# Optimization experiments

Hardware: AMD Instinct MI355X
Metric: run time of the kernel (lower is better)

The kernel has to match this reference:

```python
import jax, jax.numpy as jnp
import numpy as np

N_NODES = 100000
HID = 128
N_EDGES = 600000


def sage_conv(h, src, dst, Wl, bl, Wr, n_nodes):
    # PyG SAGEConv (mean aggr): out = lin_l(mean_{j->i} h_j) + lin_r(h_i)
    msgs = h[src]                                               # [E, d] gather
    agg = jax.ops.segment_sum(msgs, dst, num_segments=n_nodes)  # [N, d]
    cnt = jax.ops.segment_sum(jnp.ones((src.shape[0], 1), h.dtype), dst,
                              num_segments=n_nodes)             # [N, 1]
    mean = agg / jnp.maximum(cnt, 1.0)                          # isolated nodes -> 0
    return mean @ Wl.T + bl + h @ Wr.T


def setup_inputs() -> dict:
    key = jax.random.key(0)
    ks = jax.random.split(key, 8)
    scale = 1.0 / np.sqrt(HID)
    x = jnp.arange(N_NODES, dtype=jnp.int64) if jax.config.jax_enable_x64 else jnp.arange(N_NODES, dtype=jnp.int32)
    edge_index = jax.random.randint(ks[0], (2, N_EDGES), 0, N_NODES)
    emb = jax.random.normal(ks[1], (N_NODES, HID), dtype=jnp.float32) * scale
    Wl1 = jax.random.normal(ks[2], (HID, HID), dtype=jnp.float32) * scale
    bl1 = jnp.zeros((HID,), jnp.float32)
    Wr1 = jax.random.normal(ks[3], (HID, HID), dtype=jnp.float32) * scale
    Wl2 = jax.random.normal(ks[4], (HID, HID), dtype=jnp.float32) * scale
    bl2 = jnp.zeros((HID,), jnp.float32)
    Wr2 = jax.random.normal(ks[5], (HID, HID), dtype=jnp.float32) * scale
    return {"x": x, "edge_index": edge_index, "emb": emb,
            "Wl1": Wl1, "bl1": bl1, "Wr1": Wr1,
            "Wl2": Wl2, "bl2": bl2, "Wr2": Wr2}


def reference(x, edge_index, emb, Wl1, bl1, Wr1, Wl2, bl2, Wr2):
    src, dst = edge_index[0], edge_index[1]
    n = emb.shape[0]
    h = emb[x]                                          # embedding lookup [N, d]
    h = jax.nn.relu(sage_conv(h, src, dst, Wl1, bl1, Wr1, n))  # dropout = eval identity
    h = jax.nn.relu(sage_conv(h, src, dst, Wl2, bl2, Wr2, n))
    return h
```

## Files before the change

### kernel.cpp

```cpp
#include <hip/hip_runtime.h>

#define HID 128

typedef unsigned short ushort_t;
typedef unsigned int uint_t;
typedef float f32x4 __attribute__((ext_vector_type(4)));
typedef short s16x8 __attribute__((ext_vector_type(8)));

__device__ __forceinline__ ushort_t f2bf(float f) {
  uint_t u = __float_as_uint(f);
  uint_t r = (u + 0x7FFFu + ((u >> 16) & 1u)) >> 16;
  return (ushort_t)r;
}
__device__ __forceinline__ float bfLo(uint_t v) { return __uint_as_float(v << 16); }
__device__ __forceinline__ float bfHi(uint_t v) { return __uint_as_float(v & 0xFFFF0000u); }

__global__ __launch_bounds__(256) void prep_kernel(
    const float* __restrict__ emb, const int* __restrict__ x,
    ushort_t* __restrict__ hb, int N,
    const float* __restrict__ Wl1, const float* __restrict__ Wr1,
    const float* __restrict__ Wl2, const float* __restrict__ Wr2,
    ushort_t* __restrict__ wsw,
    const int* __restrict__ dst, int* __restrict__ deg, int E) {
  int tid = blockIdx.x * 256 + threadIdx.x;
  int gthreads = N * 32;
  if (tid < gthreads) {
    int r = tid >> 5, j = (tid & 31) * 4;
    int s = x[r];
    float4 v = *(const float4*)&emb[(size_t)s * HID + j];
    uint2 p;
    p.x = (uint_t)f2bf(v.x) | ((uint_t)f2bf(v.y) << 16);
    p.y = (uint_t)f2bf(v.z) | ((uint_t)f2bf(v.w) << 16);
    *(uint2*)&hb[(size_t)r * HID + j] = p;
    return;
  }
  tid -= gthreads;
  if (tid < 65536) {
    const float* srcs[4] = {Wl1, Wr1, Wl2, Wr2};
    int m = tid >> 14, idx = tid & 16383;
    int j = idx & 7;
    int lane = (idx >> 3) & 63;
    int nt = (idx >> 9) & 7;
    int ks = (idx >> 12) & 3;
    int row = nt * 16 + (lane & 15);
    int col = ks * 32 + (lane >> 4) * 8 + j;
    wsw[tid] = f2bf(srcs[m][row * HID + col]);
    return;
  }
  tid -= 65536;
  if (tid < E) atomicAdd(&deg[dst[tid]], 1);
}

__global__ __launch_bounds__(256) void scan1_kernel(
    const int* __restrict__ deg, int* __restrict__ offsets,
    int* __restrict__ sums, int N) {
  __shared__ int s[256];
  int b = blockIdx.x, t = threadIdx.x;
  int base = b * 1024 + t * 4;
  int v0 = 0, v1 = 0, v2 = 0, v3 = 0;
  if (base + 0 < N) v0 = deg[base + 0];
  if (base + 1 < N) v1 = deg[base + 1];
  if (base + 2 < N) v2 = deg[base + 2];
  if (base + 3 < N) v3 = deg[base + 3];
  int mySum = v0 + v1 + v2 + v3;
  s[t] = mySum;
  __syncthreads();
  for (int off = 1; off < 256; off <<= 1) {
    int v = (t >= off) ? s[t - off] : 0;
    __syncthreads();
    s[t] += v;
    __syncthreads();
  }
  int excl = s[t] - mySum;
  if (t == 255) sums[b] = s[255];
  if (base + 0 < N) offsets[base + 0] = excl;
  if (base + 1 < N) offsets[base + 1] = excl + v0;
  if (base + 2 < N) offsets[base + 2] = excl + v0 + v1;
  if (base + 3 < N) offsets[base + 3] = excl + v0 + v1 + v2;
}

__global__ __launch_bounds__(256) void scan3_kernel(
    int* __restrict__ offsets, const int* __restrict__ sums,
    int* __restrict__ cursor, int N, int E, int nb) {
  __shared__ int red[256];
  int t = threadIdx.x;
  int chunk = (blockIdx.x * 256) >> 10;
  red[t] = (t < chunk) ? sums[t] : 0;
  __syncthreads();
  for (int off = 128; off > 0; off >>= 1) {
    if (t < off) red[t] += red[t + off];
    __syncthreads();
  }
  int prefix = red[0];
  int i = blockIdx.x * 256 + t;
  if (i < N) {
    int v = offsets[i] + prefix;
    offsets[i] = v;
    cursor[i] = v;
  } else if (i == N) {
    offsets[N] = E;
  }
}

__global__ __launch_bounds__(256) void fill_kernel(
    const int* __restrict__ src, const int* __restrict__ dst,
    int* __restrict__ cursor, int* __restrict__ csr, int E) {
  int e = blockIdx.x * 256 + threadIdx.x;
  if (e >= E) return;
  int d = dst[e];
  int pos = atomicAdd(&cursor[d], 1);
  csr[pos] = src[e];
}

__global__ __launch_bounds__(256) void aggregate_kernel(
    const ushort_t* __restrict__ hb, const int* __restrict__ offsets,
    const int* __restrict__ csr, ushort_t* __restrict__ meanb, int N) {
  int t = threadIdx.x;
  int node = blockIdx.x * 4 + (t >> 6);
  if (node >= N) return;
  int lane = t & 63;
  int grp = lane >> 4;
  int l16 = lane & 15;
  int o0 = offsets[node], o1 = offsets[node + 1];

  float acc[8];
#pragma unroll
  for (int i = 0; i < 8; i++) acc[i] = 0.f;

  int e = o0 + grp;
  for (; e + 4 < o1; e += 8) {
    int s0 = csr[e];
    int s1 = csr[e + 4];
    uint4 v0 = *(const uint4*)&hb[(size_t)s0 * HID + l16 * 8];
    uint4 v1 = *(const uint4*)&hb[(size_t)s1 * HID + l16 * 8];
    acc[0] += bfLo(v0.x) + bfLo(v1.x);
    acc[1] += bfHi(v0.x) + bfHi(v1.x);
    acc[2] += bfLo(v0.y) + bfLo(v1.y);
    acc[3] += bfHi(v0.y) + bfHi(v1.y);
    acc[4] += bfLo(v0.z) + bfLo(v1.z);
    acc[5] += bfHi(v0.z) + bfHi(v1.z);
    acc[6] += bfLo(v0.w) + bfLo(v1.w);
    acc[7] += bfHi(v0.w) + bfHi(v1.w);
  }
  if (e < o1) {
    int s0 = csr[e];
    uint4 v0 = *(const uint4*)&hb[(size_t)s0 * HID + l16 * 8];
    acc[0] += bfLo(v0.x); acc[1] += bfHi(v0.x);
    acc[2] += bfLo(v0.y); acc[3] += bfHi(v0.y);
    acc[4] += bfLo(v0.z); acc[5] += bfHi(v0.z);
    acc[6] += bfLo(v0.w); acc[7] += bfHi(v0.w);
  }

#pragma unroll
  for (int i = 0; i < 8; i++) {
    acc[i] += __shfl_xor(acc[i], 16, 64);
    acc[i] += __shfl_xor(acc[i], 32, 64);
  }

  if (grp == 0) {
    int d = o1 - o0;
    float inv = 1.0f / (float)(d > 1 ? d : 1);
    uint4 p;
    p.x = (uint_t)f2bf(acc[0] * inv) | ((uint_t)f2bf(acc[1] * inv) << 16);
    p.y = (uint_t)f2bf(acc[2] * inv) | ((uint_t)f2bf(acc[3] * inv) << 16);
    p.z = (uint_t)f2bf(acc[4] * inv) | ((uint_t)f2bf(acc[5] * inv) << 16);
    p.w = (uint_t)f2bf(acc[6] * inv) | ((uint_t)f2bf(acc[7] * inv) << 16);
    *(uint4*)&meanb[(size_t)node * HID + l16 * 8] = p;
  }
}

__global__ __launch_bounds__(256) void mfma_gemm_kernel(
    const ushort_t* __restrict__ meanb, const ushort_t* __restrict__ hb,
    const ushort_t* __restrict__ WlS, const ushort_t* __restrict__ WrS,
    const float* __restrict__ bias, float* __restrict__ outF,
    ushort_t* __restrict__ outB, int N, int outIsBf16) {
  __shared__ ushort_t ws[32768];
  const int t = threadIdx.x;
  const int wave = t >> 6;
  const int lane = t & 63;
  const int rowBase = (blockIdx.x * 4 + wave) * 32;
  const int l15 = lane & 15;
  const int quad = lane >> 4;
  const int kq = quad * 8;
  const bool active = rowBase < N;

  int r0 = rowBase + l15;       if (r0 >= N) r0 = N - 1;
  int r1 = rowBase + 16 + l15;  if (r1 >= N) r1 = N - 1;

  s16x8 a[2][2][4];
  if (active) {
#pragma unroll
    for (int ks = 0; ks < 4; ks++) {
      a[0][0][ks] = *(const s16x8*)&meanb[(size_t)r0 * HID + ks * 32 + kq];
      a[0][1][ks] = *(const s16x8*)&meanb[(size_t)r1 * HID + ks * 32 + kq];
      a[1][0][ks] = *(const s16x8*)&hb[(size_t)r0 * HID + ks * 32 + kq];
      a[1][1][ks] = *(const s16x8*)&hb[(size_t)r1 * HID + ks * 32 + kq];
    }
  }

#pragma unroll
  for (int it = 0; it < 8; it++) {
    int o = (it * 256 + t) * 8;
    *(s16x8*)&ws[o] = *(const s16x8*)&WlS[o];
    *(s16x8*)&ws[16384 + o] = *(const s16x8*)&WrS[o];
  }
  __syncthreads();

  if (active) {
    f32x4 acc[2][8];
#pragma unroll
    for (int mt = 0; mt < 2; mt++)
#pragma unroll
      for (int nt = 0; nt < 8; nt++) acc[mt][nt] = (f32x4){0.f, 0.f, 0.f, 0.f};

#pragma unroll
    for (int half = 0; half < 2; half++) {
      const int hbase = half * 16384;
#pragma unroll
      for (int ks = 0; ks < 4; ks++)
#pragma unroll
        for (int nt = 0; nt < 8; nt++) {
          s16x8 b = *(const s16x8*)&ws[hbase + ((ks * 8 + nt) * 64 + lane) * 8];
          acc[0][nt] = __builtin_amdgcn_mfma_f32_16x16x32_bf16(a[half][0][ks], b, acc[0][nt], 0, 0, 0);
          acc[1][nt] = __builtin_amdgcn_mfma_f32_16x16x32_bf16(a[half][1][ks], b, acc[1][nt], 0, 0, 0);
        }
    }

#pragma unroll
    for (int mt = 0; mt < 2; mt++) {
#pragma unroll
      for (int nt = 0; nt < 8; nt++) {
        int col = nt * 16 + l15;
        float bv = bias[col];
#pragma unroll
        for (int r = 0; r < 4; r++) {
          int row = rowBase + mt * 16 + quad * 4 + r;
          if (row < N) {
            float v = fmaxf(acc[mt][nt][r] + bv, 0.f);
            if (outIsBf16) outB[(size_t)row * HID + col] = f2bf(v);
            else           outF[(size_t)row * HID + col] = v;
          }
        }
      }
    }
  }
}

extern "C" void kernel_launch(void* const* d_in, const int* in_sizes, int n_in,
                              void* d_out, int out_size, void* d_ws, size_t ws_size,
                              hipStream_t stream) {
  const int* x = (const int*)d_in[0];
  const int* ei = (const int*)d_in[1];
  const float* emb = (const float*)d_in[2];
  const float* Wl1 = (const float*)d_in[3];
  const float* bl1 = (const float*)d_in[4];
  const float* Wr1 = (const float*)d_in[5];
  const float* Wl2 = (const float*)d_in[6];
  const float* bl2 = (const float*)d_in[7];
  const float* Wr2 = (const float*)d_in[8];
  float* out = (float*)d_out;

  const int N = in_sizes[0];
  const int E = in_sizes[1] / 2;
  const int* srcI = ei;
  const int* dstI = ei + E;

  char* p = (char*)d_ws;
  ushort_t* hb = (ushort_t*)p;    p += (size_t)N * HID * sizeof(ushort_t);
  ushort_t* meanb = (ushort_t*)p; p += (size_t)N * HID * sizeof(ushort_t);
  ushort_t* wb = (ushort_t*)p;    p += (size_t)4 * 16384 * sizeof(ushort_t);
  int* deg = (int*)p;             p += (size_t)((N + 3) & ~3) * sizeof(int);
  int* offsets = (int*)p;         p += (size_t)((N + 4) & ~3) * sizeof(int);
  int* cursor = (int*)p;          p += (size_t)((N + 3) & ~3) * sizeof(int);
  int* csr = (int*)p;             p += (size_t)((E + 3) & ~3) * sizeof(int);
  int* sums = (int*)p;            p += 256 * sizeof(int);

  ushort_t* Wlb1 = wb;
  ushort_t* Wrb1 = wb + 16384;
  ushort_t* Wlb2 = wb + 32768;
  ushort_t* Wrb2 = wb + 49152;

  const int nScanBlocks = (N + 1023) / 1024;
  const int eBlocks = (E + 255) / 256;
  const int gemmBlocks = (N + 127) / 128;
  const int aggBlocks = (N + 3) / 4;
  const int prepBlocks = (N * 32 + 65536 + E + 255) / 256;

  hipMemsetAsync(deg, 0, (size_t)N * sizeof(int), stream);
  prep_kernel<<<prepBlocks, 256, 0, stream>>>(emb, x, hb, N,
                                              Wl1, Wr1, Wl2, Wr2, wb,
                                              dstI, deg, E);
  scan1_kernel<<<nScanBlocks, 256, 0, stream>>>(deg, offsets, sums, N);
  scan3_kernel<<<(N + 256) / 256, 256, 0, stream>>>(offsets, sums, cursor,
                                                    N, E, nScanBlocks);
  fill_kernel<<<eBlocks, 256, 0, stream>>>(srcI, dstI, cursor, csr, E);

  aggregate_kernel<<<aggBlocks, 256, 0, stream>>>(hb, offsets, csr, meanb, N);
  mfma_gemm_kernel<<<gemmBlocks, 256, 0, stream>>>(meanb, hb, Wlb1, Wrb1, bl1,
                                                   nullptr, hb, N, 1);

  aggregate_kernel<<<aggBlocks, 256, 0, stream>>>(hb, offsets, csr, meanb, N);
  mfma_gemm_kernel<<<gemmBlocks, 256, 0, stream>>>(meanb, hb, Wlb2, Wrb2, bl2,
                                                   out, nullptr, N, 0);
}
```

Measured before the change: 311.1 us.

## Fuse neighbor-mean aggregation into the per-layer MFMA GEMM kernel

Merges the aggregation and GEMM kernels into one per-layer kernel: each wave gathers the neighbor mean for its 32 rows into a swizzled LDS tile, then runs the Wl MFMA from LDS, reloads Wr into the same LDS buffer and runs the self-term MFMA. This removes the global write and re-read of the intermediate mean buffer and one launch per layer, and ping-pongs between two hidden buffers. The cost is much less parallelism in the gather phase, since each wave now walks 32 nodes serially instead of one wave per node, plus extra barriers around the weight reload. The embedding prep also moves to 8 elements per thread.

```diff
diff --git a/kernel.cpp b/kernel.cpp
--- a/kernel.cpp
+++ b/kernel.cpp
@@ -23,15 +23,19 @@
     ushort_t* __restrict__ wsw,
     const int* __restrict__ dst, int* __restrict__ deg, int E) {
   int tid = blockIdx.x * 256 + threadIdx.x;
-  int gthreads = N * 32;
+  int gthreads = N * 16;
   if (tid < gthreads) {
-    int r = tid >> 5, j = (tid & 31) * 4;
+    int r = tid >> 4, j = (tid & 15) * 8;
     int s = x[r];
-    float4 v = *(const float4*)&emb[(size_t)s * HID + j];
-    uint2 p;
-    p.x = (uint_t)f2bf(v.x) | ((uint_t)f2bf(v.y) << 16);
-    p.y = (uint_t)f2bf(v.z) | ((uint_t)f2bf(v.w) << 16);
-    *(uint2*)&hb[(size_t)r * HID + j] = p;
+    const float* src = &emb[(size_t)s * HID + j];
+    float4 v0 = *(const float4*)src;
+    float4 v1 = *(const float4*)(src + 4);
+    uint4 p;
+    p.x = (uint_t)f2bf(v0.x) | ((uint_t)f2bf(v0.y) << 16);
+    p.y = (uint_t)f2bf(v0.z) | ((uint_t)f2bf(v0.w) << 16);
+    p.z = (uint_t)f2bf(v1.x) | ((uint_t)f2bf(v1.y) << 16);
+    p.w = (uint_t)f2bf(v1.z) | ((uint_t)f2bf(v1.w) << 16);
+    *(uint4*)&hb[(size_t)r * HID + j] = p;
     return;
   }
   tid -= gthreads;
@@ -112,119 +116,128 @@
   csr[pos] = src[e];
 }
 
-__global__ __launch_bounds__(256) void aggregate_kernel(
-    const ushort_t* __restrict__ hb, const int* __restrict__ offsets,
-    const int* __restrict__ csr, ushort_t* __restrict__ meanb, int N) {
-  int t = threadIdx.x;
-  int node = blockIdx.x * 4 + (t >> 6);
-  if (node >= N) return;
-  int lane = t & 63;
-  int grp = lane >> 4;
-  int l16 = lane & 15;
-  int o0 = offsets[node], o1 = offsets[node + 1];
-
-  float acc[8];
-#pragma unroll
-  for (int i = 0; i < 8; i++) acc[i] = 0.f;
-
-  int e = o0 + grp;
-  for (; e + 4 < o1; e += 8) {
-    int s0 = csr[e];
-    int s1 = csr[e + 4];
-    uint4 v0 = *(const uint4*)&hb[(size_t)s0 * HID + l16 * 8];
-    uint4 v1 = *(const uint4*)&hb[(size_t)s1 * HID + l16 * 8];
-    acc[0] += bfLo(v0.x) + bfLo(v1.x);
-    acc[1] += bfHi(v0.x) + bfHi(v1.x);
-    acc[2] += bfLo(v0.y) + bfLo(v1.y);
-    acc[3] += bfHi(v0.y) + bfHi(v1.y);
-    acc[4] += bfLo(v0.z) + bfLo(v1.z);
-    acc[5] += bfHi(v0.z) + bfHi(v1.z);
-    acc[6] += bfLo(v0.w) + bfLo(v1.w);
-    acc[7] += bfHi(v0.w) + bfHi(v1.w);
-  }
-  if (e < o1) {
-    int s0 = csr[e];
-    uint4 v0 = *(const uint4*)&hb[(size_t)s0 * HID + l16 * 8];
-    acc[0] += bfLo(v0.x); acc[1] += bfHi(v0.x);
-    acc[2] += bfLo(v0.y); acc[3] += bfHi(v0.y);
-    acc[4] += bfLo(v0.z); acc[5] += bfHi(v0.z);
-    acc[6] += bfLo(v0.w); acc[7] += bfHi(v0.w);
-  }
-
-#pragma unroll
-  for (int i = 0; i < 8; i++) {
-    acc[i] += __shfl_xor(acc[i], 16, 64);
-    acc[i] += __shfl_xor(acc[i], 32, 64);
-  }
-
-  if (grp == 0) {
-    int d = o1 - o0;
-    float inv = 1.0f / (float)(d > 1 ? d : 1);
-    uint4 p;
-    p.x = (uint_t)f2bf(acc[0] * inv) | ((uint_t)f2bf(acc[1] * inv) << 16);
-    p.y = (uint_t)f2bf(acc[2] * inv) | ((uint_t)f2bf(acc[3] * inv) << 16);
-    p.z = (uint_t)f2bf(acc[4] * inv) | ((uint_t)f2bf(acc[5] * inv) << 16);
-    p.w = (uint_t)f2bf(acc[6] * inv) | ((uint_t)f2bf(acc[7] * inv) << 16);
-    *(uint4*)&meanb[(size_t)node * HID + l16 * 8] = p;
-  }
-}
-
-__global__ __launch_bounds__(256) void mfma_gemm_kernel(
-    const ushort_t* __restrict__ meanb, const ushort_t* __restrict__ hb,
-    const ushort_t* __restrict__ WlS, const ushort_t* __restrict__ WrS,
-    const float* __restrict__ bias, float* __restrict__ outF,
-    ushort_t* __restrict__ outB, int N, int outIsBf16) {
-  __shared__ ushort_t ws[32768];
+__global__ __launch_bounds__(256) void fused_layer_kernel(
+    const ushort_t* __restrict__ hin, const int* __restrict__ offsets,
+    const int* __restrict__ csr, const ushort_t* __restrict__ WlS,
+    const ushort_t* __restrict__ WrS, const float* __restrict__ bias,
+    float* __restrict__ outF, ushort_t* __restrict__ outB,
+    int N, int outIsBf16) {
+  __shared__ ushort_t ws[16384];
+  __shared__ ushort_t meanT[16384];
   const int t = threadIdx.x;
   const int wave = t >> 6;
   const int lane = t & 63;
   const int rowBase = (blockIdx.x * 4 + wave) * 32;
   const int l15 = lane & 15;
   const int quad = lane >> 4;
-  const int kq = quad * 8;
   const bool active = rowBase < N;
-
-  int r0 = rowBase + l15;       if (r0 >= N) r0 = N - 1;
-  int r1 = rowBase + 16 + l15;  if (r1 >= N) r1 = N - 1;
-
-  s16x8 a[2][2][4];
-  if (active) {
-#pragma unroll
-    for (int ks = 0; ks < 4; ks++) {
-      a[0][0][ks] = *(const s16x8*)&meanb[(size_t)r0 * HID + ks * 32 + kq];
-      a[0][1][ks] = *(const s16x8*)&meanb[(size_t)r1 * HID + ks * 32 + kq];
-      a[1][0][ks] = *(const s16x8*)&hb[(size_t)r0 * HID + ks * 32 + kq];
-      a[1][1][ks] = *(const s16x8*)&hb[(size_t)r1 * HID + ks * 32 + kq];
-    }
-  }
 
 #pragma unroll
   for (int it = 0; it < 8; it++) {
     int o = (it * 256 + t) * 8;
     *(s16x8*)&ws[o] = *(const s16x8*)&WlS[o];
-    *(s16x8*)&ws[16384 + o] = *(const s16x8*)&WrS[o];
-  }
-  __syncthreads();
+  }
 
   if (active) {
-    f32x4 acc[2][8];
-#pragma unroll
-    for (int mt = 0; mt < 2; mt++)
-#pragma unroll
-      for (int nt = 0; nt < 8; nt++) acc[mt][nt] = (f32x4){0.f, 0.f, 0.f, 0.f};
-
-#pragma unroll
-    for (int half = 0; half < 2; half++) {
-      const int hbase = half * 16384;
-#pragma unroll
-      for (int ks = 0; ks < 4; ks++)
-#pragma unroll
-        for (int nt = 0; nt < 8; nt++) {
-          s16x8 b = *(const s16x8*)&ws[hbase + ((ks * 8 + nt) * 64 + lane) * 8];
-          acc[0][nt] = __builtin_amdgcn_mfma_f32_16x16x32_bf16(a[half][0][ks], b, acc[0][nt], 0, 0, 0);
-          acc[1][nt] = __builtin_amdgcn_mfma_f32_16x16x32_bf16(a[half][1][ks], b, acc[1][nt], 0, 0, 0);
-        }
+    for (int nl = 0; nl < 32; nl++) {
+      int node = rowBase + nl;
+      if (node >= N) break;
+      int o0 = offsets[node], o1 = offsets[node + 1];
+      float acc[8];
+#pragma unroll
+      for (int i = 0; i < 8; i++) acc[i] = 0.f;
+      int e = o0 + quad;
+      for (; e + 4 < o1; e += 8) {
+        int s0 = csr[e];
+        int s1 = csr[e + 4];
+        uint4 v0 = *(const uint4*)&hin[(size_t)s0 * HID + l15 * 8];
+        uint4 v1 = *(const uint4*)&hin[(size_t)s1 * HID + l15 * 8];
+        acc[0] += bfLo(v0.x) + bfLo(v1.x);
+        acc[1] += bfHi(v0.x) + bfHi(v1.x);
+        acc[2] += bfLo(v0.y) + bfLo(v1.y);
+        acc[3] += bfHi(v0.y) + bfHi(v1.y);
+        acc[4] += bfLo(v0.z) + bfLo(v1.z);
+        acc[5] += bfHi(v0.z) + bfHi(v1.z);
+        acc[6] += bfLo(v0.w) + bfLo(v1.w);
+        acc[7] += bfHi(v0.w) + bfHi(v1.w);
+      }
+      if (e < o1) {
+        int s0 = csr[e];
+        uint4 v0 = *(const uint4*)&hin[(size_t)s0 * HID + l15 * 8];
+        acc[0] += bfLo(v0.x); acc[1] += bfHi(v0.x);
+        acc[2] += bfLo(v0.y); acc[3] += bfHi(v0.y);
+        acc[4] += bfLo(v0.z); acc[5] += bfHi(v0.z);
+        acc[6] += bfLo(v0.w); acc[7] += bfHi(v0.w);
+      }
+#pragma unroll
+      for (int i = 0; i < 8; i++) {
+        acc[i] += __shfl_xor(acc[i], 16, 64);
+        acc[i] += __shfl_xor(acc[i], 32, 64);
+      }
+      if (quad == 0) {
+        int d = o1 - o0;
+        float inv = 1.0f / (float)(d > 1 ? d : 1);
+        uint4 p;
+        p.x = (uint_t)f2bf(acc[0] * inv) | ((uint_t)f2bf(acc[1] * inv) << 16);
+        p.y = (uint_t)f2bf(acc[2] * inv) | ((uint_t)f2bf(acc[3] * inv) << 16);
+        p.z = (uint_t)f2bf(acc[4] * inv) | ((uint_t)f2bf(acc[5] * inv) << 16);
+        p.w = (uint_t)f2bf(acc[6] * inv) | ((uint_t)f2bf(acc[7] * inv) << 16);
+        *(uint4*)&meanT[((wave * 32 + nl) * 16 + (l15 ^ (nl & 7))) * 8] = p;
+      }
     }
+  }
+
+  s16x8 ah[2][4];
+  if (active) {
+    int r0 = rowBase + l15;       if (r0 >= N) r0 = N - 1;
+    int r1 = rowBase + 16 + l15;  if (r1 >= N) r1 = N - 1;
+#pragma unroll
+    for (int ks = 0; ks < 4; ks++) {
+      ah[0][ks] = *(const s16x8*)&hin[(size_t)r0 * HID + ks * 32 + quad * 8];
+      ah[1][ks] = *(const s16x8*)&hin[(size_t)r1 * HID + ks * 32 + quad * 8];
+    }
+  }
+
+  __syncthreads();
+
+  f32x4 acc[2][8];
+#pragma unroll
+  for (int mt = 0; mt < 2; mt++)
+#pragma unroll
+    for (int nt = 0; nt < 8; nt++) acc[mt][nt] = (f32x4){0.f, 0.f, 0.f, 0.f};
+
+  if (active) {
+#pragma unroll
+    for (int ks = 0; ks < 4; ks++) {
+      int c = (ks * 4 + quad);
+      s16x8 a0 = *(const s16x8*)&meanT[((wave * 32 + l15) * 16 + (c ^ (l15 & 7))) * 8];
+      s16x8 a1 = *(const s16x8*)&meanT[((wave * 32 + 16 + l15) * 16 + (c ^ (l15 & 7))) * 8];
+#pragma unroll
+      for (int nt = 0; nt < 8; nt++) {
+        s16x8 b = *(const s16x8*)&ws[((ks * 8 + nt) * 64 + lane) * 8];
+        acc[0][nt] = __builtin_amdgcn_mfma_f32_16x16x32_bf16(a0, b, acc[0][nt], 0, 0, 0);
+        acc[1][nt] = __builtin_amdgcn_mfma_f32_16x16x32_bf16(a1, b, acc[1][nt], 0, 0, 0);
+      }
+    }
+  }
+
+  __syncthreads();
+#pragma unroll
+  for (int it = 0; it < 8; it++) {
+    int o = (it * 256 + t) * 8;
+    *(s16x8*)&ws[o] = *(const s16x8*)&WrS[o];
+  }
+  __syncthreads();
+
+  if (active) {
+#pragma unroll
+    for (int ks = 0; ks < 4; ks++)
+#pragma unroll
+      for (int nt = 0; nt < 8; nt++) {
+        s16x8 b = *(const s16x8*)&ws[((ks * 8 + nt) * 64 + lane) * 8];
+        acc[0][nt] = __builtin_amdgcn_mfma_f32_16x16x32_bf16(ah[0][ks], b, acc[0][nt], 0, 0, 0);
+        acc[1][nt] = __builtin_amdgcn_mfma_f32_16x16x32_bf16(ah[1][ks], b, acc[1][nt], 0, 0, 0);
+      }
 
 #pragma unroll
     for (int mt = 0; mt < 2; mt++) {
@@ -267,7 +280,7 @@
 
   char* p = (char*)d_ws;
   ushort_t* hb = (ushort_t*)p;    p += (size_t)N * HID * sizeof(ushort_t);
-  ushort_t* meanb = (ushort_t*)p; p += (size_t)N * HID * sizeof(ushort_t);
+  ushort_t* h2 = (ushort_t*)p;    p += (size_t)N * HID * sizeof(ushort_t);
   ushort_t* wb = (ushort_t*)p;    p += (size_t)4 * 16384 * sizeof(ushort_t);
   int* deg = (int*)p;             p += (size_t)((N + 3) & ~3) * sizeof(int);
   int* offsets = (int*)p;         p += (size_t)((N + 4) & ~3) * sizeof(int);
@@ -282,9 +295,8 @@
 
   const int nScanBlocks = (N + 1023) / 1024;
   const int eBlocks = (E + 255) / 256;
-  const int gemmBlocks = (N + 127) / 128;
-  const int aggBlocks = (N + 3) / 4;
-  const int prepBlocks = (N * 32 + 65536 + E + 255) / 256;
+  const int layerBlocks = (N + 127) / 128;
+  const int prepBlocks = (N * 16 + 65536 + E + 255) / 256;
 
   hipMemsetAsync(deg, 0, (size_t)N * sizeof(int), stream);
   prep_kernel<<<prepBlocks, 256, 0, stream>>>(emb, x, hb, N,
@@ -295,11 +307,9 @@
                                                     N, E, nScanBlocks);
   fill_kernel<<<eBlocks, 256, 0, stream>>>(srcI, dstI, cursor, csr, E);
 
-  aggregate_kernel<<<aggBlocks, 256, 0, stream>>>(hb, offsets, csr, meanb, N);
-  mfma_gemm_kernel<<<gemmBlocks, 256, 0, stream>>>(meanb, hb, Wlb1, Wrb1, bl1,
-                                                   nullptr, hb, N, 1);
-
-  aggregate_kernel<<<aggBlocks, 256, 0, stream>>>(hb, offsets, csr, meanb, N);
-  mfma_gemm_kernel<<<gemmBlocks, 256, 0, stream>>>(meanb, hb, Wlb2, Wrb2, bl2,
-                                                   out, nullptr, N, 0);
-}
+  fused_layer_kernel<<<layerBlocks, 256, 0, stream>>>(
+      hb, offsets, csr, Wlb1, Wrb1, bl1, nullptr, h2, N, 1);
+
+  fused_layer_kernel<<<layerBlocks, 256, 0, stream>>>(
+      h2, offsets, csr, Wlb2, Wrb2, bl2, out, nullptr, N, 0);
+}
```

Result: slower. 434.5 us (+39.7%).
